# Kernel optimization log

Measured on AMD Instinct MI355X. Metric: run time of the kernel, lower is better.

The kernel has to match this reference:

```python
import jax, jax.numpy as jnp
import numpy as np


def _lstm_layer(x, w_ih, w_hh, b_ih, b_hh):
    # x: [B,T,I]; w_ih: [4H,I]; w_hh: [4H,H]. PyTorch gate order: i,f,g,o.
    B, T, _ = x.shape
    H = w_hh.shape[1]
    xg = jnp.einsum('bti,gi->btg', x, w_ih) + b_ih  # precompute input gates [B,T,4H]

    def step(carry, xt):
        h, c = carry
        g = xt + h @ w_hh.T + b_hh
        i, f, gg, o = jnp.split(g, 4, axis=-1)
        c = jax.nn.sigmoid(f) * c + jax.nn.sigmoid(i) * jnp.tanh(gg)
        h = jax.nn.sigmoid(o) * jnp.tanh(c)
        return (h, c), h

    init = (jnp.zeros((B, H), x.dtype), jnp.zeros((B, H), x.dtype))
    _, hs = jax.lax.scan(step, init, jnp.swapaxes(xg, 0, 1))  # [T,B,H]
    return jnp.swapaxes(hs, 0, 1)


def _lstm2(x, p):  # 2-layer stacked LSTM; p = list of 2 layer param tuples
    for (wih, whh, bih, bhh) in p:
        x = _lstm_layer(x, wih, whh, bih, bhh)
    return x


def setup_inputs() -> dict:
    key = jax.random.key(0)
    ks = iter(jax.random.split(key, 32))
    d = {'x': jax.random.normal(next(ks), (100, 75, 75), jnp.float32)}
    specs = {
        'w_ih_1_0': (512, 75), 'w_hh_1_0': (512, 128), 'b_ih_1_0': (512,), 'b_hh_1_0': (512,),
        'w_ih_1_1': (512, 128), 'w_hh_1_1': (512, 128), 'b_ih_1_1': (512,), 'b_hh_1_1': (512,),
        'w_ih_2_0': (256, 128), 'w_hh_2_0': (256, 64), 'b_ih_2_0': (256,), 'b_hh_2_0': (256,),
        'w_ih_2_1': (256, 64), 'w_hh_2_1': (256, 64), 'b_ih_2_1': (256,), 'b_hh_2_1': (256,),
        'w_ih_3_0': (128, 64), 'w_hh_3_0': (128, 32), 'b_ih_3_0': (128,), 'b_hh_3_0': (128,),
        'w_ih_3_1': (128, 32), 'w_hh_3_1': (128, 32), 'b_ih_3_1': (128,), 'b_hh_3_1': (128,),
        'lin_w': (60, 2400), 'lin_b': (60,),
    }
    for name, shp in specs.items():
        d[name] = jax.random.normal(next(ks), shp, jnp.float32) * 0.1
    return d


def reference(x,
              w_ih_1_0, w_hh_1_0, b_ih_1_0, b_hh_1_0,
              w_ih_1_1, w_hh_1_1, b_ih_1_1, b_hh_1_1,
              w_ih_2_0, w_hh_2_0, b_ih_2_0, b_hh_2_0,
              w_ih_2_1, w_hh_2_1, b_ih_2_1, b_hh_2_1,
              w_ih_3_0, w_hh_3_0, b_ih_3_0, b_hh_3_0,
              w_ih_3_1, w_hh_3_1, b_ih_3_1, b_hh_3_1,
              lin_w, lin_b):
    x = _lstm2(x, [(w_ih_1_0, w_hh_1_0, b_ih_1_0, b_hh_1_0),
                   (w_ih_1_1, w_hh_1_1, b_ih_1_1, b_hh_1_1)])
    x = _lstm2(x, [(w_ih_2_0, w_hh_2_0, b_ih_2_0, b_hh_2_0),
                   (w_ih_2_1, w_hh_2_1, b_ih_2_1, b_hh_2_1)])
    x = _lstm2(x, [(w_ih_3_0, w_hh_3_0, b_ih_3_0, b_hh_3_0),
                   (w_ih_3_1, w_hh_3_1, b_ih_3_1, b_hh_3_1)])
    x = x.reshape((100, 32 * 75))  # [B, T*H] (row-major, matches torch)
    return x @ lin_w.T + lin_b
```

## Files before the change

### kernel.cpp

```cpp
#include <hip/hip_runtime.h>

using half8 = __attribute__((ext_vector_type(8))) _Float16;
using f32x4 = __attribute__((ext_vector_type(4))) float;

__device__ __forceinline__ float sigmf(float x) {
    return __builtin_amdgcn_rcpf(1.0f + __expf(-x));
}
__device__ __forceinline__ float tanhx(float x) {
    return 1.0f - 2.0f * __builtin_amdgcn_rcpf(1.0f + __expf(x + x));
}

struct PrepPtrs {
    const float* wih[6];
    const float* whh[6];
    const float* bi[6];
    const float* bh[6];
    const float* x;
    _Float16* wihI0;
    _Float16* wihI1;
    _Float16* wihI2;
    _Float16* wihP3;
    _Float16* wihP4;
    _Float16* wihP5;
    _Float16* whhP[6];
    float* biasI;
    float* biasP;
    _Float16* x16;
};

__global__ __launch_bounds__(256) void prep_kernel(PrepPtrs p) {
    int i = blockIdx.x * 256 + threadIdx.x;
    if (i < 642048) {
        int row = i / 76, k = i - row * 76;
        int t = row / 112, b = row - t * 112;
        float v = (b < 100 && k < 75 && t < 75)
                      ? p.x[((size_t)b * 75 + t) * 75 + k]
                      : 0.0f;
        p.x16[i] = (_Float16)v;
        return;
    }
    i -= 642048;
    if (i < 38912) {
        int n = i / 76, k = i - n * 76;
        int col = n >> 2, G = n & 3;
        float v = (k < 75) ? p.wih[0][(size_t)(G * 128 + col) * 75 + k] : 0.0f;
        p.wihI0[i] = (_Float16)v;
        return;
    }
    i -= 38912;
    if (i < 65536) {
        int n = i >> 7, k = i & 127;
        int col = n >> 2, G = n & 3;
        p.wihI1[i] = (_Float16)p.wih[1][(size_t)(G * 128 + col) * 128 + k];
        return;
    }
    i -= 65536;
    if (i < 32768) {
        int n = i >> 7, k = i & 127;
        int col = n >> 2, G = n & 3;
        p.wihI2[i] = (_Float16)p.wih[2][(size_t)(G * 64 + col) * 128 + k];
        return;
    }
    i -= 32768;
    if (i < 16384) { p.wihP3[i] = (_Float16)p.wih[3][i]; return; }
    i -= 16384;
    if (i < 8192) { p.wihP4[i] = (_Float16)p.wih[4][i]; return; }
    i -= 8192;
    if (i < 4096) { p.wihP5[i] = (_Float16)p.wih[5][i]; return; }
    i -= 4096;
    constexpr int WHHC[6] = {65536, 65536, 16384, 16384, 4096, 4096};
    #pragma unroll
    for (int l = 0; l < 6; ++l) {
        if (i < WHHC[l]) { p.whhP[l][i] = (_Float16)p.whh[l][i]; return; }
        i -= WHHC[l];
    }
    constexpr int BIH[3] = {128, 128, 64};
    constexpr int BIO[3] = {0, 512, 1024};
    #pragma unroll
    for (int j = 0; j < 3; ++j) {
        int cnt = 4 * BIH[j];
        if (i < cnt) {
            int col = i >> 2, G = i & 3;
            int src = G * BIH[j] + col;
            p.biasI[BIO[j] + i] = p.bi[j][src] + p.bh[j][src];
            return;
        }
        i -= cnt;
    }
    if (i < 256) { p.biasP[i] = p.bi[3][i] + p.bh[3][i]; return; }
    i -= 256;
    if (i < 128) { p.biasP[256 + i] = p.bi[4][i] + p.bh[4][i]; return; }
    i -= 128;
    if (i < 128) { p.biasP[384 + i] = p.bi[5][i] + p.bh[5][i]; return; }
}

template <int Ks>
__global__ __launch_bounds__(256) void gemm_xg(
    const _Float16* __restrict__ A, const _Float16* __restrict__ W,
    const float* __restrict__ bias, float* __restrict__ C, int Kv, int N) {
    constexpr int KP = Ks * 32;
    constexpr int LDK = KP + 8;
    __shared__ __align__(16) _Float16 Al[64][LDK];
    __shared__ __align__(16) _Float16 Wl[64][LDK];

    const int tid = threadIdx.x;
    const int tt = blockIdx.x >> 1;
    const int boff = (blockIdx.x & 1) * 48;
    const int n0 = blockIdx.y * 64;
    constexpr int HP = KP / 2;

    for (int idx = tid; idx < 64 * HP; idx += 256) {
        int row = idx / HP;
        int k = (idx - row * HP) * 2;
        unsigned int va = 0, vw = 0;
        if (k < Kv) {
            va = *(const unsigned int*)(A + (size_t)(tt * 112 + boff + row) * Kv + k);
            vw = *(const unsigned int*)(W + (size_t)(n0 + row) * Kv + k);
        }
        *(unsigned int*)&Al[row][k] = va;
        *(unsigned int*)&Wl[row][k] = vw;
    }
    __syncthreads();

    const int w = tid >> 6, l = tid & 63, hi = l >> 4;
    half8 a[Ks];
    #pragma unroll
    for (int kk = 0; kk < Ks; ++kk)
        a[kk] = *(const half8*)&Al[w * 16 + (l & 15)][kk * 32 + hi * 8];

    f32x4 acc[4];
    #pragma unroll
    for (int jt = 0; jt < 4; ++jt) {
        acc[jt] = f32x4{0.f, 0.f, 0.f, 0.f};
        #pragma unroll
        for (int kk = 0; kk < Ks; ++kk) {
            half8 b = *(const half8*)&Wl[jt * 16 + (l & 15)][kk * 32 + hi * 8];
            acc[jt] = __builtin_amdgcn_mfma_f32_16x16x32_f16(a[kk], b, acc[jt], 0, 0, 0);
        }
    }

    const int bx = (boff >> 2) + w * 4 + hi;
    #pragma unroll
    for (int jt = 0; jt < 4; ++jt) {
        int n = n0 + jt * 16 + (l & 15);
        float bs = bias[n];
        f32x4 v = acc[jt];
        v[0] += bs; v[1] += bs; v[2] += bs; v[3] += bs;
        *(f32x4*)(C + ((size_t)(tt * 28 + bx) * N + n) * 4) = v;
    }
}

#define FTAIL                                                                 \
    __builtin_amdgcn_sched_barrier(0);                                        \
    asm volatile("s_waitcnt lgkmcnt(0)");                                     \
    __builtin_amdgcn_sched_barrier(0);                                        \
    __builtin_amdgcn_s_barrier();                                             \
    __builtin_amdgcn_sched_barrier(0);

#define PICK(A4) ((hi & 2) ? ((hi & 1) ? A4[3] : A4[2]) : ((hi & 1) ? A4[1] : A4[0]))

#define ACT(aI, aF, aG4, aO)                                                  \
    float gI = PICK(aI), gF = PICK(aF), gG = PICK(aG4), gO = PICK(aO);        \
    float si = sigmf(gI), sf = sigmf(gF), tg = tanhx(gG), so = sigmf(gO);     \
    float cn = sf * cst + si * tg;                                            \
    cst = cn;                                                                 \
    float hn = so * tanhx(cn);                                                \
    _Float16 hv = (_Float16)hn;

template <int H>
__global__ __launch_bounds__(4 * H) void lstm_rec(
    const float* __restrict__ xg, const _Float16* __restrict__ whh,
    _Float16* __restrict__ hout) {
    constexpr int Ks = H / 32;
    constexpr int LDH = H + 8;
    constexpr int XSTR = 448 * H;
    constexpr int HSTR = 112 * H;

    __shared__ __align__(16) _Float16 hbuf[2][4][LDH];

    const int tid = threadIdx.x;
    const int w = tid >> 6, l = tid & 63, hi = l >> 4;
    const int col = w * 16 + (l & 15);
    const int blk = blockIdx.x;

    half8 bw[4][Ks];
    #pragma unroll
    for (int G = 0; G < 4; ++G)
        #pragma unroll
        for (int kk = 0; kk < Ks; ++kk)
            bw[G][kk] = *(const half8*)(whh + (size_t)(G * H + col) * H + kk * 32 + hi * 8);

    for (int i = tid; i < 2 * 4 * LDH; i += 4 * H) ((_Float16*)hbuf)[i] = (_Float16)0;
    __syncthreads();

    const float* xp = xg + (size_t)blk * (4 * H * 4) + col * 16;
    _Float16* hop = hout + (size_t)(blk * 4 + hi) * H + col;

    f32x4 P0[4], P1[4], P2[4];
#define XLOAD(PA)                                                             \
    PA[0] = *(const f32x4*)(xp + 0);                                          \
    PA[1] = *(const f32x4*)(xp + 4);                                          \
    PA[2] = *(const f32x4*)(xp + 8);                                          \
    PA[3] = *(const f32x4*)(xp + 12);                                         \
    xp += XSTR;

    XLOAD(P0)
    XLOAD(P1)
    XLOAD(P2)

    float cst = 0.f;

#define LSTM_STEP(PA, CUR)                                                    \
    {                                                                         \
        half8 afr[Ks];                                                        \
        _Pragma("unroll") for (int kk = 0; kk < Ks; ++kk)                     \
            afr[kk] = *(const half8*)&hbuf[CUR][(l & 15) & 3][kk * 32 + hi * 8]; \
        f32x4 aI = PA[0], aF = PA[1], aG4 = PA[2], aO = PA[3];                \
        XLOAD(PA)                                                             \
        _Pragma("unroll") for (int kk = 0; kk < Ks; ++kk) {                   \
            aI = __builtin_amdgcn_mfma_f32_16x16x32_f16(afr[kk], bw[0][kk], aI, 0, 0, 0);  \
            aF = __builtin_amdgcn_mfma_f32_16x16x32_f16(afr[kk], bw[1][kk], aF, 0, 0, 0);  \
            aG4 = __builtin_amdgcn_mfma_f32_16x16x32_f16(afr[kk], bw[2][kk], aG4, 0, 0, 0);\
            aO = __builtin_amdgcn_mfma_f32_16x16x32_f16(afr[kk], bw[3][kk], aO, 0, 0, 0);  \
        }                                                                     \
        ACT(aI, aF, aG4, aO)                                                  \
        hbuf[CUR ^ 1][hi][col] = hv;                                          \
        *hop = hv;                                                            \
        hop += HSTR;                                                          \
        FTAIL                                                                 \
    }

    #pragma unroll 1
    for (int it = 0; it < 12; ++it) {
        LSTM_STEP(P0, 0) LSTM_STEP(P1, 1) LSTM_STEP(P2, 0)
        LSTM_STEP(P0, 1) LSTM_STEP(P1, 0) LSTM_STEP(P2, 1)
    }
    LSTM_STEP(P0, 0) LSTM_STEP(P1, 1) LSTM_STEP(P2, 0)
#undef LSTM_STEP
#undef XLOAD
}

__global__ __launch_bounds__(768) void lstm_quad(
    const float* __restrict__ xg,
    const _Float16* __restrict__ whh2, const _Float16* __restrict__ whh3,
    const _Float16* __restrict__ wih3, const _Float16* __restrict__ whh4,
    const _Float16* __restrict__ wih4, const _Float16* __restrict__ whh5,
    const _Float16* __restrict__ wih5, const float* __restrict__ biasP,
    _Float16* __restrict__ hout) {
    __shared__ __align__(16) _Float16 hb2[2][4][72], hp2[2][4][72];
    __shared__ __align__(16) _Float16 hb3[2][4][72], hp3[2][4][72];
    __shared__ __align__(16) _Float16 hb4[2][4][40], hp4[2][4][40];
    __shared__ __align__(16) _Float16 hb5[2][4][40];

    const int tid = threadIdx.x;
    const int w = tid >> 6, l = tid & 63, hi = l >> 4;
    const int lr = (l & 15) & 3;
    const int blk = blockIdx.x;

    for (int i = tid; i < 2 * 4 * 72; i += 768) {
        ((_Float16*)hb2)[i] = (_Float16)0; ((_Float16*)hp2)[i] = (_Float16)0;
        ((_Float16*)hb3)[i] = (_Float16)0; ((_Float16*)hp3)[i] = (_Float16)0;
    }
    for (int i = tid; i < 2 * 4 * 40; i += 768) {
        ((_Float16*)hb4)[i] = (_Float16)0; ((_Float16*)hp4)[i] = (_Float16)0;
        ((_Float16*)hb5)[i] = (_Float16)0;
    }
    __syncthreads();

    float cst = 0.f;

    if (w < 4) {
        const int col = w * 16 + (l & 15);
        half8 bw[4][2];
        #pragma unroll
        for (int G = 0; G < 4; ++G)
            #pragma unroll
            for (int kk = 0; kk < 2; ++kk)
                bw[G][kk] = *(const half8*)(whh2 + (size_t)(G * 64 + col) * 64 + kk * 32 + hi * 8);
        const float* xp = xg + (size_t)blk * 1024 + col * 16;
        f32x4 P0[4], P1[4], P2[4];
#define XLOADQ(PA)                                                            \
        PA[0] = *(const f32x4*)(xp + 0);                                      \
        PA[1] = *(const f32x4*)(xp + 4);                                      \
        PA[2] = *(const f32x4*)(xp + 8);                                      \
        PA[3] = *(const f32x4*)(xp + 12);                                     \
        xp += 28672;
        XLOADQ(P0)
        XLOADQ(P1)
        XLOADQ(P2)

#define QA(PA, CUR, S)                                                        \
        {                                                                     \
            if ((S) < 75) {                                                   \
                half8 afr[2];                                                 \
                _Pragma("unroll") for (int kk = 0; kk < 2; ++kk)              \
                    afr[kk] = *(const half8*)&hb2[CUR][lr][kk * 32 + hi * 8]; \
                f32x4 aI = PA[0], aF = PA[1], aG4 = PA[2], aO = PA[3];        \
                XLOADQ(PA)                                                    \
                _Pragma("unroll") for (int kk = 0; kk < 2; ++kk) {            \
                    aI = __builtin_amdgcn_mfma_f32_16x16x32_f16(afr[kk], bw[0][kk], aI, 0, 0, 0);  \
                    aF = __builtin_amdgcn_mfma_f32_16x16x32_f16(afr[kk], bw[1][kk], aF, 0, 0, 0);  \
                    aG4 = __builtin_amdgcn_mfma_f32_16x16x32_f16(afr[kk], bw[2][kk], aG4, 0, 0, 0);\
                    aO = __builtin_amdgcn_mfma_f32_16x16x32_f16(afr[kk], bw[3][kk], aO, 0, 0, 0);  \
                }                                                             \
                ACT(aI, aF, aG4, aO)                                          \
                hb2[(CUR) ^ 1][hi][col] = hv;                                 \
                hp2[(CUR) ^ 1][hi][col] = hv;                                 \
            }                                                                 \
            FTAIL                                                             \
        }
        #pragma unroll 1
        for (int it = 0; it < 13; ++it) {
            const int b6 = it * 6;
            QA(P0, 0, b6 + 0) QA(P1, 1, b6 + 1) QA(P2, 0, b6 + 2)
            QA(P0, 1, b6 + 3) QA(P1, 0, b6 + 4) QA(P2, 1, b6 + 5)
        }
#undef QA
#undef XLOADQ
    } else if (w < 8) {
        const int col = (w - 4) * 16 + (l & 15);
        half8 bwB[4][2], bwI[4][2];
        #pragma unroll
        for (int G = 0; G < 4; ++G)
            #pragma unroll
            for (int kk = 0; kk < 2; ++kk) {
                bwB[G][kk] = *(const half8*)(whh3 + (size_t)(G * 64 + col) * 64 + kk * 32 + hi * 8);
                bwI[G][kk] = *(const half8*)(wih3 + (size_t)(G * 64 + col) * 64 + kk * 32 + hi * 8);
            }
        const float bI = biasP[col], bF = biasP[64 + col];
        const float bG = biasP[128 + col], bO = biasP[192 + col];
        #pragma unroll 1
        for (int s = 0; s < 78; ++s) {
            const int cur = s & 1;
            if (s >= 1 && s <= 75) {
                half8 afr[2], air[2];
                #pragma unroll
                for (int kk = 0; kk < 2; ++kk) {
                    afr[kk] = *(const half8*)&hb3[cur][lr][kk * 32 + hi * 8];
                    air[kk] = *(const half8*)&hp2[cur][lr][kk * 32 + hi * 8];
                }
                f32x4 aI = {bI, bI, bI, bI}, aF = {bF, bF, bF, bF};
                f32x4 aG4 = {bG, bG, bG, bG}, aO = {bO, bO, bO, bO};
                #pragma unroll
                for (int kk = 0; kk < 2; ++kk) {
                    aI = __builtin_amdgcn_mfma_f32_16x16x32_f16(afr[kk], bwB[0][kk], aI, 0, 0, 0);
                    aF = __builtin_amdgcn_mfma_f32_16x16x32_f16(afr[kk], bwB[1][kk], aF, 0, 0, 0);
                    aG4 = __builtin_amdgcn_mfma_f32_16x16x32_f16(afr[kk], bwB[2][kk], aG4, 0, 0, 0);
                    aO = __builtin_amdgcn_mfma_f32_16x16x32_f16(afr[kk], bwB[3][kk], aO, 0, 0, 0);
                }
                #pragma unroll
                for (int kk = 0; kk < 2; ++kk) {
                    aI = __builtin_amdgcn_mfma_f32_16x16x32_f16(air[kk], bwI[0][kk], aI, 0, 0, 0);
                    aF = __builtin_amdgcn_mfma_f32_16x16x32_f16(air[kk], bwI[1][kk], aF, 0, 0, 0);
                    aG4 = __builtin_amdgcn_mfma_f32_16x16x32_f16(air[kk], bwI[2][kk], aG4, 0, 0, 0);
                    aO = __builtin_amdgcn_mfma_f32_16x16x32_f16(air[kk], bwI[3][kk], aO, 0, 0, 0);
                }
                ACT(aI, aF, aG4, aO)
                hb3[cur ^ 1][hi][col] = hv;
                hp3[cur ^ 1][hi][col] = hv;
            }
            FTAIL
        }
    } else if (w < 10) {
        const int col = (w - 8) * 16 + (l & 15);
        half8 bwB[4], bwI[4][2];
        #pragma unroll
        for (int G = 0; G < 4; ++G) {
            bwB[G] = *(const half8*)(whh4 + (size_t)(G * 32 + col) * 32 + hi * 8);
            #pragma unroll
            for (int kk = 0; kk < 2; ++kk)
                bwI[G][kk] = *(const half8*)(wih4 + (size_t)(G * 32 + col) * 64 + kk * 32 + hi * 8);
        }
        const float* bp = biasP + 256;
        const float bI = bp[col], bF = bp[32 + col], bG = bp[64 + col], bO = bp[96 + col];
        #pragma unroll 1
        for (int s = 0; s < 78; ++s) {
            const int cur = s & 1;
            if (s >= 2 && s <= 76) {
                half8 afr = *(const half8*)&hb4[cur][lr][hi * 8];
                half8 air[2];
                #pragma unroll
                for (int kk = 0; kk < 2; ++kk)
                    air[kk] = *(const half8*)&hp3[cur][lr][kk * 32 + hi * 8];
                f32x4 aI = {bI, bI, bI, bI}, aF = {bF, bF, bF, bF};
                f32x4 aG4 = {bG, bG, bG, bG}, aO = {bO, bO, bO, bO};
                aI = __builtin_amdgcn_mfma_f32_16x16x32_f16(afr, bwB[0], aI, 0, 0, 0);
                aF = __builtin_amdgcn_mfma_f32_16x16x32_f16(afr, bwB[1], aF, 0, 0, 0);
                aG4 = __builtin_amdgcn_mfma_f32_16x16x32_f16(afr, bwB[2], aG4, 0, 0, 0);
                aO = __builtin_amdgcn_mfma_f32_16x16x32_f16(afr, bwB[3], aO, 0, 0, 0);
                #pragma unroll
                for (int kk = 0; kk < 2; ++kk) {
                    aI = __builtin_amdgcn_mfma_f32_16x16x32_f16(air[kk], bwI[0][kk], aI, 0, 0, 0);
                    aF = __builtin_amdgcn_mfma_f32_16x16x32_f16(air[kk], bwI[1][kk], aF, 0, 0, 0);
                    aG4 = __builtin_amdgcn_mfma_f32_16x16x32_f16(air[kk], bwI[2][kk], aG4, 0, 0, 0);
                    aO = __builtin_amdgcn_mfma_f32_16x16x32_f16(air[kk], bwI[3][kk], aO, 0, 0, 0);
                }
                ACT(aI, aF, aG4, aO)
                hb4[cur ^ 1][hi][col] = hv;
                hp4[cur ^ 1][hi][col] = hv;
            }
            FTAIL
        }
    } else {
        const int col = (w - 10) * 16 + (l & 15);
        half8 bwB[4], bwI[4];
        #pragma unroll
        for (int G = 0; G < 4; ++G) {
            bwB[G] = *(const half8*)(whh5 + (size_t)(G * 32 + col) * 32 + hi * 8);
            bwI[G] = *(const half8*)(wih5 + (size_t)(G * 32 + col) * 32 + hi * 8);
        }
        const float* bp = biasP + 384;
        const float bI = bp[col], bF = bp[32 + col], bG = bp[64 + col], bO = bp[96 + col];
        _Float16* hop = hout + (size_t)(blk * 4 + hi) * 32 + col;
        #pragma unroll 1
        for (int s = 0; s < 78; ++s) {
            const int cur = s & 1;
            if (s >= 3) {
                half8 afr = *(const half8*)&hb5[cur][lr][hi * 8];
                half8 air = *(const half8*)&hp4[cur][lr][hi * 8];
                f32x4 aI = {bI, bI, bI, bI}, aF = {bF, bF, bF, bF};
                f32x4 aG4 = {bG, bG, bG, bG}, aO = {bO, bO, bO, bO};
                aI = __builtin_amdgcn_mfma_f32_16x16x32_f16(afr, bwB[0], aI, 0, 0, 0);
                aF = __builtin_amdgcn_mfma_f32_16x16x32_f16(afr, bwB[1], aF, 0, 0, 0);
                aG4 = __builtin_amdgcn_mfma_f32_16x16x32_f16(afr, bwB[2], aG4, 0, 0, 0);
                aO = __builtin_amdgcn_mfma_f32_16x16x32_f16(afr, bwB[3], aO, 0, 0, 0);
                aI = __builtin_amdgcn_mfma_f32_16x16x32_f16(air, bwI[0], aI, 0, 0, 0);
                aF = __builtin_amdgcn_mfma_f32_16x16x32_f16(air, bwI[1], aF, 0, 0, 0);
                aG4 = __builtin_amdgcn_mfma_f32_16x16x32_f16(air, bwI[2], aG4, 0, 0, 0);
                aO = __builtin_amdgcn_mfma_f32_16x16x32_f16(air, bwI[3], aO, 0, 0, 0);
                ACT(aI, aF, aG4, aO)
                hb5[cur ^ 1][hi][col] = hv;
                *hop = hv;
                hop += 3584;
            }
            FTAIL
        }
    }
}

__global__ __launch_bounds__(256) void linear_out(
    const _Float16* __restrict__ h, const float* __restrict__ lw,
    const float* __restrict__ lb, float* __restrict__ out) {
    int wave = (blockIdx.x * 256 + threadIdx.x) >> 6;
    int l = threadIdx.x & 63;
    if (wave >= 6000) return;
    int b = wave / 60, o = wave - b * 60;
    int hc = l & 31, t0 = l >> 5;
    float acc = 0.f;
    for (int t = t0; t < 75; t += 2)
        acc += (float)h[((size_t)t * 112 + b) * 32 + hc] * lw[(size_t)o * 2400 + t * 32 + hc];
    #pragma unroll
    for (int s = 32; s; s >>= 1) acc += __shfl_xor(acc, s, 64);
    if (l == 0) out[b * 60 + o] = acc + lb[o];
}

extern "C" void kernel_launch(void* const* d_in, const int* in_sizes, int n_in,
                              void* d_out, int out_size, void* d_ws, size_t ws_size,
                              hipStream_t stream) {
    const float* x = (const float*)d_in[0];
    const float* wih[6];
    const float* whhp[6];
    const float* bih[6];
    const float* bhh[6];
    for (int i = 0; i < 6; ++i) {
        wih[i] = (const float*)d_in[1 + 4 * i];
        whhp[i] = (const float*)d_in[2 + 4 * i];
        bih[i] = (const float*)d_in[3 + 4 * i];
        bhh[i] = (const float*)d_in[4 + 4 * i];
    }
    const float* lw = (const float*)d_in[25];
    const float* lb = (const float*)d_in[26];
    float* out = (float*)d_out;

    char* ws = (char*)d_ws;
    size_t cur = 0;
    auto alloc = [&](size_t b) {
        size_t o = cur;
        cur += (b + 255) & ~(size_t)255;
        return o;
    };
    _Float16* x16 = (_Float16*)(ws + alloc((size_t)8448 * 76 * 2));
    _Float16* wihI0 = (_Float16*)(ws + alloc(38912 * 2));
    _Float16* wihI1 = (_Float16*)(ws + alloc(65536 * 2));
    _Float16* wihI2 = (_Float16*)(ws + alloc(32768 * 2));
    _Float16* wihP3 = (_Float16*)(ws + alloc(16384 * 2));
    _Float16* wihP4 = (_Float16*)(ws + alloc(8192 * 2));
    _Float16* wihP5 = (_Float16*)(ws + alloc(4096 * 2));
    _Float16* whhP[6];
    const size_t whhBytes[6] = {131072, 131072, 32768, 32768, 8192, 8192};
    for (int i = 0; i < 6; ++i) whhP[i] = (_Float16*)(ws + alloc(whhBytes[i]));
    float* biasI = (float*)(ws + alloc(1280 * 4));
    float* biasP = (float*)(ws + alloc(512 * 4));
    float* xg = (float*)(ws + alloc((size_t)78 * 28 * 512 * 4 * 4));
    _Float16* h0 = (_Float16*)(ws + alloc((size_t)75 * 112 * 128 * 2));
    _Float16* h1 = (_Float16*)(ws + alloc((size_t)75 * 112 * 128 * 2));
    _Float16* h5 = (_Float16*)(ws + alloc((size_t)75 * 112 * 32 * 2));

    PrepPtrs pp;
    for (int i = 0; i < 6; ++i) {
        pp.wih[i] = wih[i];
        pp.whh[i] = whhp[i];
        pp.bi[i] = bih[i];
        pp.bh[i] = bhh[i];
        pp.whhP[i] = whhP[i];
    }
    pp.x = x;
    pp.wihI0 = wihI0;
    pp.wihI1 = wihI1;
    pp.wihI2 = wihI2;
    pp.wihP3 = wihP3;
    pp.wihP4 = wihP4;
    pp.wihP5 = wihP5;
    pp.biasI = biasI;
    pp.biasP = biasP;
    pp.x16 = x16;
    prep_kernel<<<3835, 256, 0, stream>>>(pp);

    gemm_xg<3><<<dim3(150, 8), 256, 0, stream>>>(x16, wihI0, biasI + 0, xg, 76, 512);
    lstm_rec<128><<<25, 512, 0, stream>>>(xg, whhP[0], h0);
    gemm_xg<4><<<dim3(150, 8), 256, 0, stream>>>(h0, wihI1, biasI + 512, xg, 128, 512);
    lstm_rec<128><<<25, 512, 0, stream>>>(xg, whhP[1], h1);
    gemm_xg<4><<<dim3(150, 4), 256, 0, stream>>>(h1, wihI2, biasI + 1024, xg, 128, 256);
    lstm_quad<<<25, 768, 0, stream>>>(xg, whhP[2], whhP[3], wihP3, whhP[4],
                                      wihP4, whhP[5], wihP5, biasP, h5);

    linear_out<<<1500, 256, 0, stream>>>(h5, lw, lb, out);
}
```

Before: 187.1 us.

## Fuse final linear into lstm_quad and convert x inline in first GEMM

Adds a 13th wave to lstm_quad that accumulates the output linear layer with MFMA from the last layer's hidden states in shared memory, using an fp16 repacked weight prepared in prep_kernel. This removes the separate linear_out launch and the h5 global round trip. The first input GEMM now reads fp32 x directly and converts it to fp16 while loading, removing the x16 conversion pass from prep. It costs an extra wave sharing the per-step barriers in the recurrent kernel, plus uncoalesced scalar loads in gemm_xg0.

```diff
diff --git a/kernel.cpp b/kernel.cpp
--- a/kernel.cpp
+++ b/kernel.cpp
@@ -15,7 +15,7 @@
     const float* whh[6];
     const float* bi[6];
     const float* bh[6];
-    const float* x;
+    const float* lw;
     _Float16* wihI0;
     _Float16* wihI1;
     _Float16* wihI2;
@@ -25,21 +25,11 @@
     _Float16* whhP[6];
     float* biasI;
     float* biasP;
-    _Float16* x16;
+    _Float16* lwI;
 };
 
 __global__ __launch_bounds__(256) void prep_kernel(PrepPtrs p) {
     int i = blockIdx.x * 256 + threadIdx.x;
-    if (i < 642048) {
-        int row = i / 76, k = i - row * 76;
-        int t = row / 112, b = row - t * 112;
-        float v = (b < 100 && k < 75 && t < 75)
-                      ? p.x[((size_t)b * 75 + t) * 75 + k]
-                      : 0.0f;
-        p.x16[i] = (_Float16)v;
-        return;
-    }
-    i -= 642048;
     if (i < 38912) {
         int n = i / 76, k = i - n * 76;
         int col = n >> 2, G = n & 3;
@@ -74,6 +64,16 @@
         if (i < WHHC[l]) { p.whhP[l][i] = (_Float16)p.whh[l][i]; return; }
         i -= WHHC[l];
     }
+    if (i < 153600) {
+        int t = i >> 11;
+        int rem = i & 2047;
+        int tile = rem >> 9, op = (rem >> 5) & 15, hc = rem & 31;
+        int o = tile * 16 + op;
+        float v = (o < 60) ? p.lw[(size_t)o * 2400 + t * 32 + hc] : 0.0f;
+        p.lwI[i] = (_Float16)v;
+        return;
+    }
+    i -= 153600;
     constexpr int BIH[3] = {128, 128, 64};
     constexpr int BIO[3] = {0, 512, 1024};
     #pragma unroll
@@ -92,6 +92,64 @@
     if (i < 128) { p.biasP[256 + i] = p.bi[4][i] + p.bh[4][i]; return; }
     i -= 128;
     if (i < 128) { p.biasP[384 + i] = p.bi[5][i] + p.bh[5][i]; return; }
+}
+
+__global__ __launch_bounds__(256) void gemm_xg0(
+    const float* __restrict__ X,
+    const _Float16* __restrict__ W,
+    const float* __restrict__ bias, float* __restrict__ C) {
+    constexpr int Ks = 3, KP = 96, LDK = 104, HP = 48, Kv = 76, N = 512;
+    __shared__ __align__(16) _Float16 Al[64][LDK];
+    __shared__ __align__(16) _Float16 Wl[64][LDK];
+
+    const int tid = threadIdx.x;
+    const int tt = blockIdx.x >> 1;
+    const int boff = (blockIdx.x & 1) * 48;
+    const int n0 = blockIdx.y * 64;
+
+    for (int idx = tid; idx < 64 * HP; idx += 256) {
+        int row = idx / HP;
+        int k = (idx - row * HP) * 2;
+        unsigned int va = 0, vw = 0;
+        int b = boff + row;
+        if (b < 100 && k < 75) {
+            float f0 = X[((size_t)b * 75 + tt) * 75 + k];
+            float f1 = (k + 1 < 75) ? X[((size_t)b * 75 + tt) * 75 + k + 1] : 0.0f;
+            _Float16 h2[2] = {(_Float16)f0, (_Float16)f1};
+            va = *(unsigned int*)h2;
+        }
+        if (k < Kv) vw = *(const unsigned int*)(W + (size_t)(n0 + row) * Kv + k);
+        *(unsigned int*)&Al[row][k] = va;
+        *(unsigned int*)&Wl[row][k] = vw;
+    }
+    __syncthreads();
+
+    const int w = tid >> 6, l = tid & 63, hi = l >> 4;
+    half8 a[Ks];
+    #pragma unroll
+    for (int kk = 0; kk < Ks; ++kk)
+        a[kk] = *(const half8*)&Al[w * 16 + (l & 15)][kk * 32 + hi * 8];
+
+    f32x4 acc[4];
+    #pragma unroll
+    for (int jt = 0; jt < 4; ++jt) {
+        acc[jt] = f32x4{0.f, 0.f, 0.f, 0.f};
+        #pragma unroll
+        for (int kk = 0; kk < Ks; ++kk) {
+            half8 b = *(const half8*)&Wl[jt * 16 + (l & 15)][kk * 32 + hi * 8];
+            acc[jt] = __builtin_amdgcn_mfma_f32_16x16x32_f16(a[kk], b, acc[jt], 0, 0, 0);
+        }
+    }
+
+    const int bx = (boff >> 2) + w * 4 + hi;
+    #pragma unroll
+    for (int jt = 0; jt < 4; ++jt) {
+        int n = n0 + jt * 16 + (l & 15);
+        float bs = bias[n];
+        f32x4 v = acc[jt];
+        v[0] += bs; v[1] += bs; v[2] += bs; v[3] += bs;
+        *(f32x4*)(C + ((size_t)(tt * 28 + bx) * N + n) * 4) = v;
+    }
 }
 
 template <int Ks>
@@ -240,13 +298,15 @@
 #undef XLOAD
 }
 
-__global__ __launch_bounds__(768) void lstm_quad(
+__global__ __launch_bounds__(832) void lstm_quad(
     const float* __restrict__ xg,
     const _Float16* __restrict__ whh2, const _Float16* __restrict__ whh3,
     const _Float16* __restrict__ wih3, const _Float16* __restrict__ whh4,
     const _Float16* __restrict__ wih4, const _Float16* __restrict__ whh5,
     const _Float16* __restrict__ wih5, const float* __restrict__ biasP,
-    _Float16* __restrict__ hout) {
+    const _Float16* __restrict__ lwI,
+    const float* __restrict__ lb,
+    float* __restrict__ outF) {
     __shared__ __align__(16) _Float16 hb2[2][4][72], hp2[2][4][72];
     __shared__ __align__(16) _Float16 hb3[2][4][72], hp3[2][4][72];
     __shared__ __align__(16) _Float16 hb4[2][4][40], hp4[2][4][40];
@@ -257,11 +317,11 @@
     const int lr = (l & 15) & 3;
     const int blk = blockIdx.x;
 
-    for (int i = tid; i < 2 * 4 * 72; i += 768) {
+    for (int i = tid; i < 2 * 4 * 72; i += 832) {
         ((_Float16*)hb2)[i] = (_Float16)0; ((_Float16*)hp2)[i] = (_Float16)0;
         ((_Float16*)hb3)[i] = (_Float16)0; ((_Float16*)hp3)[i] = (_Float16)0;
     }
-    for (int i = tid; i < 2 * 4 * 40; i += 768) {
+    for (int i = tid; i < 2 * 4 * 40; i += 832) {
         ((_Float16*)hb4)[i] = (_Float16)0; ((_Float16*)hp4)[i] = (_Float16)0;
         ((_Float16*)hb5)[i] = (_Float16)0;
     }
@@ -401,7 +461,7 @@
             }
             FTAIL
         }
-    } else {
+    } else if (w < 12) {
         const int col = (w - 10) * 16 + (l & 15);
         half8 bwB[4], bwI[4];
         #pragma unroll
@@ -411,7 +471,6 @@
         }
         const float* bp = biasP + 384;
         const float bI = bp[col], bF = bp[32 + col], bG = bp[64 + col], bO = bp[96 + col];
-        _Float16* hop = hout + (size_t)(blk * 4 + hi) * 32 + col;
         #pragma unroll 1
         for (int s = 0; s < 78; ++s) {
             const int cur = s & 1;
@@ -430,28 +489,74 @@
                 aO = __builtin_amdgcn_mfma_f32_16x16x32_f16(air, bwI[3], aO, 0, 0, 0);
                 ACT(aI, aF, aG4, aO)
                 hb5[cur ^ 1][hi][col] = hv;
-                *hop = hv;
-                hop += 3584;
             }
             FTAIL
         }
-    }
-}
-
-__global__ __launch_bounds__(256) void linear_out(
-    const _Float16* __restrict__ h, const float* __restrict__ lw,
-    const float* __restrict__ lb, float* __restrict__ out) {
-    int wave = (blockIdx.x * 256 + threadIdx.x) >> 6;
-    int l = threadIdx.x & 63;
-    if (wave >= 6000) return;
-    int b = wave / 60, o = wave - b * 60;
-    int hc = l & 31, t0 = l >> 5;
-    float acc = 0.f;
-    for (int t = t0; t < 75; t += 2)
-        acc += (float)h[((size_t)t * 112 + b) * 32 + hc] * lw[(size_t)o * 2400 + t * 32 + hc];
-    #pragma unroll
-    for (int s = 32; s; s >>= 1) acc += __shfl_xor(acc, s, 64);
-    if (l == 0) out[b * 60 + o] = acc + lb[o];
+    } else {
+        const int ln = l & 15;
+        const _Float16* lwp = lwI + (size_t)ln * 32 + hi * 8;
+        half8 LA[4], LB[4];
+        #pragma unroll
+        for (int tl = 0; tl < 4; ++tl) {
+            LA[tl] = *(const half8*)(lwp + (size_t)(0 * 4 + tl) * 512);
+            LB[tl] = *(const half8*)(lwp + (size_t)(1 * 4 + tl) * 512);
+        }
+        f32x4 acc[4];
+        #pragma unroll
+        for (int tl = 0; tl < 4; ++tl) acc[tl] = f32x4{0.f, 0.f, 0.f, 0.f};
+
+        #pragma unroll 1
+        for (int it = 0; it < 39; ++it) {
+            {
+                int t = 2 * it - 4;
+                if (t >= 0) {
+                    half8 hf = *(const half8*)&hb5[0][lr][hi * 8];
+                    #pragma unroll
+                    for (int tl = 0; tl < 4; ++tl)
+                        acc[tl] = __builtin_amdgcn_mfma_f32_16x16x32_f16(LA[tl], hf, acc[tl], 0, 0, 0);
+                }
+                int tn = t + 2;
+                if (tn < 0) tn = 0;
+                if (tn > 74) tn = 74;
+                #pragma unroll
+                for (int tl = 0; tl < 4; ++tl)
+                    LA[tl] = *(const half8*)(lwp + ((size_t)tn * 4 + tl) * 512);
+                FTAIL
+            }
+            {
+                int t = 2 * it - 3;
+                if (t >= 0) {
+                    half8 hf = *(const half8*)&hb5[1][lr][hi * 8];
+                    #pragma unroll
+                    for (int tl = 0; tl < 4; ++tl)
+                        acc[tl] = __builtin_amdgcn_mfma_f32_16x16x32_f16(LB[tl], hf, acc[tl], 0, 0, 0);
+                }
+                int tn = t + 2;
+                if (tn < 0) tn = 0;
+                if (tn > 74) tn = 74;
+                #pragma unroll
+                for (int tl = 0; tl < 4; ++tl)
+                    LB[tl] = *(const half8*)(lwp + ((size_t)tn * 4 + tl) * 512);
+                FTAIL
+            }
+        }
+        {
+            half8 hf = *(const half8*)&hb5[0][lr][hi * 8];
+            #pragma unroll
+            for (int tl = 0; tl < 4; ++tl)
+                acc[tl] = __builtin_amdgcn_mfma_f32_16x16x32_f16(LA[tl], hf, acc[tl], 0, 0, 0);
+        }
+        if (ln < 4) {
+            int b = blk * 4 + ln;
+            #pragma unroll
+            for (int tl = 0; tl < 4; ++tl)
+                #pragma unroll
+                for (int r = 0; r < 4; ++r) {
+                    int o = tl * 16 + hi * 4 + r;
+                    if (o < 60) outF[b * 60 + o] = acc[tl][r] + lb[o];
+                }
+        }
+    }
 }
 
 extern "C" void kernel_launch(void* const* d_in, const int* in_sizes, int n_in,
@@ -479,7 +584,6 @@
         cur += (b + 255) & ~(size_t)255;
         return o;
     };
-    _Float16* x16 = (_Float16*)(ws + alloc((size_t)8448 * 76 * 2));
     _Float16* wihI0 = (_Float16*)(ws + alloc(38912 * 2));
     _Float16* wihI1 = (_Float16*)(ws + alloc(65536 * 2));
     _Float16* wihI2 = (_Float16*)(ws + alloc(32768 * 2));
@@ -489,12 +593,12 @@
     _Float16* whhP[6];
     const size_t whhBytes[6] = {131072, 131072, 32768, 32768, 8192, 8192};
     for (int i = 0; i < 6; ++i) whhP[i] = (_Float16*)(ws + alloc(whhBytes[i]));
+    _Float16* lwI = (_Float16*)(ws + alloc(153600 * 2));
     float* biasI = (float*)(ws + alloc(1280 * 4));
     float* biasP = (float*)(ws + alloc(512 * 4));
     float* xg = (float*)(ws + alloc((size_t)78 * 28 * 512 * 4 * 4));
     _Float16* h0 = (_Float16*)(ws + alloc((size_t)75 * 112 * 128 * 2));
     _Float16* h1 = (_Float16*)(ws + alloc((size_t)75 * 112 * 128 * 2));
-    _Float16* h5 = (_Float16*)(ws + alloc((size_t)75 * 112 * 32 * 2));
 
     PrepPtrs pp;
     for (int i = 0; i < 6; ++i) {
@@ -504,7 +608,7 @@
         pp.bh[i] = bhh[i];
         pp.whhP[i] = whhP[i];
     }
-    pp.x = x;
+    pp.lw = lw;
     pp.wihI0 = wihI0;
     pp.wihI1 = wihI1;
     pp.wihI2 = wihI2;
@@ -513,16 +617,14 @@
     pp.wihP5 = wihP5;
     pp.biasI = biasI;
     pp.biasP = biasP;
-    pp.x16 = x16;
-    prep_kernel<<<3835, 256, 0, stream>>>(pp);
-
-    gemm_xg<3><<<dim3(150, 8), 256, 0, stream>>>(x16, wihI0, biasI + 0, xg, 76, 512);
+    pp.lwI = lwI;
+    prep_kernel<<<1927, 256, 0, stream>>>(pp);
+
+    gemm_xg0<<<dim3(150, 8), 256, 0, stream>>>(x, wihI0, biasI + 0, xg);
     lstm_rec<128><<<25, 512, 0, stream>>>(xg, whhP[0], h0);
     gemm_xg<4><<<dim3(150, 8), 256, 0, stream>>>(h0, wihI1, biasI + 512, xg, 128, 512);
     lstm_rec<128><<<25, 512, 0, stream>>>(xg, whhP[1], h1);
     gemm_xg<4><<<dim3(150, 4), 256, 0, stream>>>(h1, wihI2, biasI + 1024, xg, 128, 256);
-    lstm_quad<<<25, 768, 0, stream>>>(xg, whhP[2], whhP[3], wihP3, whhP[4],
-                                      wihP4, whhP[5], wihP5, biasP, h5);
-
-    linear_out<<<1500, 256, 0, stream>>>(h5, lw, lb, out);
-}
+    lstm_quad<<<25, 832, 0, stream>>>(xg, whhP[2], whhP[3], wihP3, whhP[4],
+                                      wihP4, whhP[5], wihP5, biasP, lwI, lb, out);
+}
```

Result: faster. 180.4 us (-3.6%).
